# Kernel tuning notes

Measured on AMD Instinct MI355X. Metric: run time of the kernel, lower is better.

## Reference

```python
import jax, jax.numpy as jnp
import numpy as np

B, C, T = 16, 768, 1024
STEPS, NNEG, OFFSET = 12, 10, 1
COPIES = NNEG + 1


def setup_inputs() -> dict:
    key = jax.random.key(0)
    k1, k2, k3, k4 = jax.random.split(key, 4)
    x = jax.random.normal(k1, (B, C, T), jnp.float32)
    y = jax.random.normal(k2, (B, C, T), jnp.float32)
    # ConvTranspose2d(in_dim, out_dim, (1, steps)) weight -> [C_in, C_out, steps]
    W = jax.random.normal(k3, (C, C, STEPS), jnp.float32) * 0.02
    b = jnp.zeros((C,), jnp.float32)
    # Negative-sample indices, replicating torch sample_negatives (sample_distance=None):
    # randint in [0, T-1), bump collisions with the positive timestep, add per-batch offset.
    neg = jax.random.randint(k4, (B, NNEG * T), 0, T - 1)
    tszs = jnp.repeat(jnp.arange(T), NNEG)  # [NNEG*T]
    neg = jnp.where(neg >= tszs[None, :], neg + 1, neg)
    neg = neg + jnp.arange(B)[:, None] * T  # index into flattened [B*T]
    return {"x": x, "y": y, "W": W, "b": b, "neg_idxs": neg}


def reference(x, y, W, b, neg_idxs):
    # project_to_steps: ConvTranspose2d with kernel (1, STEPS) on [B,C,T,1] -> [B,C,T,STEPS]
    proj = jnp.einsum('bct,cds->bdts', x, W) + b[None, :, None, None]

    # gather negatives: y -> [C, B*T], fancy-index, reshape to [NNEG, B, C, T]
    yf = jnp.transpose(y, (1, 0, 2)).reshape(C, B * T)
    negs = yf[:, neg_idxs.reshape(-1)].reshape(C, B, NNEG, T)
    negs = jnp.transpose(negs, (2, 1, 0, 3))  # [NNEG, B, C, T]

    targets = jnp.concatenate([y[None], negs], axis=0)  # [COPIES, B, C, T]

    steps = min(STEPS, T - OFFSET)
    preds = []
    for i in range(steps):  # small fixed loop over prediction steps (ragged slice sizes)
        off = i + OFFSET
        # [T-off, B, COPIES]: dot context at step i with targets shifted by off
        p = jnp.einsum('bct,nbct->tbn', proj[..., :T - off, i], targets[..., off:])
        preds.append(p.reshape(-1))
    predictions = jnp.concatenate(preds).reshape(-1, COPIES)  # infonce logits
    labels = jnp.zeros((predictions.shape[0],), jnp.int32)  # positive is copy 0
    return predictions, labels
```

## Files before the change

### kernel.cpp

```cpp
#include <hip/hip_runtime.h>

typedef __bf16 bf16;
typedef __attribute__((ext_vector_type(8))) __bf16 bf16x8;
typedef __attribute__((ext_vector_type(4))) __bf16 bf16x4;
typedef __attribute__((ext_vector_type(4))) float f32x4;

#define B_ 16
#define C_ 768
#define T_ 1024
#define S_ 12
#define NNEG_ 10
#define NCOPY 11
#define NPRED_ROWS 195360
#define NPRED (NPRED_ROWS * NCOPY)

__device__ __forceinline__ void gload16(const void* g, void* l) {
    __builtin_amdgcn_global_load_lds(
        (__attribute__((address_space(1))) void*)g,
        (__attribute__((address_space(3))) void*)l, 16, 0, 0);
}

__global__ void k_wt(const float* __restrict__ W, bf16* __restrict__ WtT) {
    int id = blockIdx.x * blockDim.x + threadIdx.x;
    if (id >= C_ * C_) return;
    int d = id / C_, c = id % C_;
    const float* src = W + ((size_t)c * C_ + d) * S_;
#pragma unroll
    for (int s = 0; s < S_; ++s)
        WtT[(size_t)s * C_ * C_ + id] = (bf16)src[s];
}

__global__ void k_tr(const float* __restrict__ src, bf16* __restrict__ dst, int b0) {
    __shared__ float tile[32][33];
    int bb = blockIdx.z;
    int b = b0 + bb;
    int c0 = blockIdx.y * 32, t0 = blockIdx.x * 32;
    int tx = threadIdx.x & 31, ty = threadIdx.x >> 5;
#pragma unroll
    for (int i = 0; i < 4; ++i)
        tile[ty + i * 8][tx] = src[((size_t)b * C_ + c0 + ty + i * 8) * T_ + t0 + tx];
    __syncthreads();
#pragma unroll
    for (int i = 0; i < 4; ++i)
        dst[((size_t)bb * T_ + t0 + ty + i * 8) * C_ + c0 + tx] = (bf16)tile[tx][ty + i * 8];
}

__global__ void k_labels(float* __restrict__ out) {
    int i = blockIdx.x * blockDim.x + threadIdx.x;
    if (i < NPRED_ROWS) out[NPRED + i] = 0.0f;
}

__global__ __launch_bounds__(256) void k_gemm(
    const bf16* __restrict__ xTc, const bf16* __restrict__ WtT,
    const float* __restrict__ bias, bf16* __restrict__ P)
{
    const int nblk = blockIdx.x;
    const int tblk = blockIdx.y;
    const int bb   = blockIdx.z;
    const int tid  = threadIdx.x;
    const int wave = tid >> 6, lane = tid & 63;
    const int mw = wave >> 1, nw = wave & 1;
    const int quad = lane >> 4, l15 = lane & 15;

    __shared__ __align__(16) bf16 sA[8][2][64][8];
    __shared__ __align__(16) bf16 sB[8][2][64][8];

    const int colk = quad * 8;
    const int rA0 = nblk * 128 + (2 * wave) * 16 + l15;
    const int rB0 = tblk * 128 + (2 * wave) * 16 + l15;
    const bf16* gA0 = WtT + (size_t)rA0 * C_ + colk;
    const bf16* gA1 = gA0 + (size_t)16 * C_;
    const bf16* gB0 = xTc + ((size_t)bb * T_ + rB0) * C_ + colk;
    const bf16* gB1 = gB0 + (size_t)16 * C_;

    f32x4 acc[4][4] = {};

    for (int k0 = 0; k0 < C_; k0 += 64) {
        __syncthreads();
        gload16(gA0 + k0,      &sA[2 * wave][0][0][0]);
        gload16(gA0 + k0 + 32, &sA[2 * wave][1][0][0]);
        gload16(gA1 + k0,      &sA[2 * wave + 1][0][0][0]);
        gload16(gA1 + k0 + 32, &sA[2 * wave + 1][1][0][0]);
        gload16(gB0 + k0,      &sB[2 * wave][0][0][0]);
        gload16(gB0 + k0 + 32, &sB[2 * wave][1][0][0]);
        gload16(gB1 + k0,      &sB[2 * wave + 1][0][0][0]);
        gload16(gB1 + k0 + 32, &sB[2 * wave + 1][1][0][0]);
        __syncthreads();

#pragma unroll
        for (int ks = 0; ks < 2; ++ks) {
            bf16x8 af[4], bfr[4];
#pragma unroll
            for (int i = 0; i < 4; ++i) af[i]  = *(const bf16x8*)&sA[mw * 4 + i][ks][lane][0];
#pragma unroll
            for (int j = 0; j < 4; ++j) bfr[j] = *(const bf16x8*)&sB[nw * 4 + j][ks][lane][0];
#pragma unroll
            for (int i = 0; i < 4; ++i)
#pragma unroll
                for (int j = 0; j < 4; ++j)
                    acc[i][j] = __builtin_amdgcn_mfma_f32_16x16x32_bf16(af[i], bfr[j], acc[i][j], 0, 0, 0);
        }
    }

#pragma unroll
    for (int i = 0; i < 4; ++i) {
        const int nb = (mw * 4 + i) * 16 + quad * 4;
        const f32x4 bv = *(const f32x4*)&bias[(nblk % 6) * 128 + nb];
#pragma unroll
        for (int j = 0; j < 4; ++j) {
            const int t = tblk * 128 + (nw * 4 + j) * 16 + l15;
            bf16x4 v;
#pragma unroll
            for (int r = 0; r < 4; ++r) v[r] = (bf16)(acc[i][j][r] + bv[r]);
            *(bf16x4*)&P[((size_t)bb * T_ + t) * (size_t)(S_ * C_) + (size_t)nblk * 128 + nb] = v;
        }
    }
}

__global__ __launch_bounds__(256) void k_pred(
    const bf16* __restrict__ P, const bf16* __restrict__ yTc,
    const int* __restrict__ neg, float* __restrict__ out, int b0)
{
    const int widx = (blockIdx.x << 2) + (threadIdx.x >> 6);
    const int lane = threadIdx.x & 63;
    const int bb = widx >> 10, tp = widx & 1023;
    const int b = b0 + bb;
    const int quad = lane >> 4, l15 = lane & 15;

    int sA = l15 < S_ ? l15 : S_ - 1;
    int tA = tp - 1 - sA;
    if (tA < 0) tA = 0;
    const bf16* arow = P + ((size_t)bb * T_ + tA) * (S_ * C_) + sA * C_ + quad * 8;

    int ridx;
    if (l15 == 0)            ridx = bb * T_ + tp;
    else if (l15 < NCOPY)    ridx = neg[(size_t)b * (NNEG_ * T_) + (l15 - 1) * T_ + tp] - b0 * T_;
    else                     ridx = bb * T_ + tp;
    const bf16* brow = yTc + (size_t)ridx * C_ + quad * 8;

    f32x4 acc = {};
#pragma unroll 4
    for (int kt = 0; kt < C_ / 32; ++kt) {
        bf16x8 av = *(const bf16x8*)(arow + kt * 32);
        bf16x8 bv = *(const bf16x8*)(brow + kt * 32);
        acc = __builtin_amdgcn_mfma_f32_16x16x32_bf16(av, bv, acc, 0, 0, 0);
    }

    if (l15 < NCOPY) {
#pragma unroll
        for (int r = 0; r < 4; ++r) {
            int s = quad * 4 + r;
            int t = tp - 1 - s;
            if (s < S_ && t >= 0) {
                int rowbase = s * (T_ - 1) - (s * (s - 1)) / 2;
                out[(((size_t)(rowbase + t)) * B_ + b) * NCOPY + l15] = acc[r];
            }
        }
    }
}

extern "C" void kernel_launch(void* const* d_in, const int* in_sizes, int n_in,
                              void* d_out, int out_size, void* d_ws, size_t ws_size,
                              hipStream_t stream) {
    const float* x    = (const float*)d_in[0];
    const float* y    = (const float*)d_in[1];
    const float* W    = (const float*)d_in[2];
    const float* bias = (const float*)d_in[3];
    const int*   neg  = (const int*)d_in[4];
    float* out = (float*)d_out;

    const size_t offW    = (size_t)S_ * C_ * C_ * 2;
    const size_t perb_xy = (size_t)T_ * C_ * 2;
    const size_t perb_p  = (size_t)T_ * S_ * C_ * 2;
    const size_t perb    = 2 * perb_xy + perb_p;

    int bchunk = (int)((ws_size - offW) / perb);
    if (bchunk < 1) bchunk = 1;
    if (bchunk > B_) bchunk = B_;

    char* ws = (char*)d_ws;
    bf16* WtT = (bf16*)ws;
    bf16* xTc = (bf16*)(ws + offW);
    bf16* yTc = (bf16*)(ws + offW + (size_t)bchunk * perb_xy);
    bf16* P   = (bf16*)(ws + offW + (size_t)bchunk * perb_xy * 2);

    k_wt<<<dim3((C_ * C_ + 255) / 256), 256, 0, stream>>>(W, WtT);
    k_labels<<<dim3((NPRED_ROWS + 255) / 256), 256, 0, stream>>>(out);

    for (int b0 = 0; b0 < B_;) {
        int cb = bchunk < (B_ - b0) ? bchunk : (B_ - b0);
        k_tr<<<dim3(T_ / 32, C_ / 32, cb), 256, 0, stream>>>(x, xTc, b0);
        k_tr<<<dim3(T_ / 32, C_ / 32, cb), 256, 0, stream>>>(y, yTc, b0);
        k_gemm<<<dim3(72, 8, cb), 256, 0, stream>>>(xTc, WtT, bias, P);
        k_pred<<<dim3(cb * 256), 256, 0, stream>>>(P, yTc, neg, out, b0);
        b0 += cb;
    }
}
```

Measured before the change: 745.2 us.

## Use 32x32x16 MFMA in projection GEMM and fuse small launches

The projection GEMM switches from 16x16x32 to 32x32x16 bf16 MFMA tiles with a 2x2 accumulator layout per wave. It halves the k-step to 32 and shrinks the LDS staging buffers to match. The two transpose launches are merged into one grid over x and y, and label zeroing moves into the prediction kernel, so k_labels is no longer launched. This removes launch overhead and aims for better MFMA throughput per LDS read, at the cost of twice as many k-loop barriers.

```diff
diff --git a/kernel.cpp b/kernel.cpp
--- a/kernel.cpp
+++ b/kernel.cpp
@@ -4,6 +4,7 @@
 typedef __attribute__((ext_vector_type(8))) __bf16 bf16x8;
 typedef __attribute__((ext_vector_type(4))) __bf16 bf16x4;
 typedef __attribute__((ext_vector_type(4))) float f32x4;
+typedef __attribute__((ext_vector_type(16))) float f32x16;
 
 #define B_ 16
 #define C_ 768
@@ -30,9 +31,13 @@
         WtT[(size_t)s * C_ * C_ + id] = (bf16)src[s];
 }
 
-__global__ void k_tr(const float* __restrict__ src, bf16* __restrict__ dst, int b0) {
+__global__ void k_tr2(const float* __restrict__ x, const float* __restrict__ y,
+                      bf16* __restrict__ xTc, bf16* __restrict__ yTc, int b0, int cb) {
     __shared__ float tile[32][33];
-    int bb = blockIdx.z;
+    int zz = blockIdx.z;
+    const float* src = (zz < cb) ? x : y;
+    bf16* dst = (zz < cb) ? xTc : yTc;
+    int bb = (zz < cb) ? zz : zz - cb;
     int b = b0 + bb;
     int c0 = blockIdx.y * 32, t0 = blockIdx.x * 32;
     int tx = threadIdx.x & 31, ty = threadIdx.x >> 5;
@@ -45,11 +50,6 @@
         dst[((size_t)bb * T_ + t0 + ty + i * 8) * C_ + c0 + tx] = (bf16)tile[tx][ty + i * 8];
 }
 
-__global__ void k_labels(float* __restrict__ out) {
-    int i = blockIdx.x * blockDim.x + threadIdx.x;
-    if (i < NPRED_ROWS) out[NPRED + i] = 0.0f;
-}
-
 __global__ __launch_bounds__(256) void k_gemm(
     const bf16* __restrict__ xTc, const bf16* __restrict__ WtT,
     const float* __restrict__ bias, bf16* __restrict__ P)
@@ -60,59 +60,53 @@
     const int tid  = threadIdx.x;
     const int wave = tid >> 6, lane = tid & 63;
     const int mw = wave >> 1, nw = wave & 1;
-    const int quad = lane >> 4, l15 = lane & 15;
+    const int l31 = lane & 31, lhi = lane >> 5;
 
-    __shared__ __align__(16) bf16 sA[8][2][64][8];
-    __shared__ __align__(16) bf16 sB[8][2][64][8];
+    __shared__ __align__(16) bf16 sA[4][2][64][8];
+    __shared__ __align__(16) bf16 sB[4][2][64][8];
 
-    const int colk = quad * 8;
-    const int rA0 = nblk * 128 + (2 * wave) * 16 + l15;
-    const int rB0 = tblk * 128 + (2 * wave) * 16 + l15;
-    const bf16* gA0 = WtT + (size_t)rA0 * C_ + colk;
-    const bf16* gA1 = gA0 + (size_t)16 * C_;
-    const bf16* gB0 = xTc + ((size_t)bb * T_ + rB0) * C_ + colk;
-    const bf16* gB1 = gB0 + (size_t)16 * C_;
+    const bf16* gA = WtT + (size_t)(nblk * 128 + wave * 32 + l31) * C_ + lhi * 8;
+    const bf16* gB = xTc + ((size_t)bb * T_ + tblk * 128 + wave * 32 + l31) * C_ + lhi * 8;
 
-    f32x4 acc[4][4] = {};
+    f32x16 acc[2][2] = {};
 
-    for (int k0 = 0; k0 < C_; k0 += 64) {
+    for (int k0 = 0; k0 < C_; k0 += 32) {
         __syncthreads();
-        gload16(gA0 + k0,      &sA[2 * wave][0][0][0]);
-        gload16(gA0 + k0 + 32, &sA[2 * wave][1][0][0]);
-        gload16(gA1 + k0,      &sA[2 * wave + 1][0][0][0]);
-        gload16(gA1 + k0 + 32, &sA[2 * wave + 1][1][0][0]);
-        gload16(gB0 + k0,      &sB[2 * wave][0][0][0]);
-        gload16(gB0 + k0 + 32, &sB[2 * wave][1][0][0]);
-        gload16(gB1 + k0,      &sB[2 * wave + 1][0][0][0]);
-        gload16(gB1 + k0 + 32, &sB[2 * wave + 1][1][0][0]);
+        gload16(gA + k0,      &sA[wave][0][0][0]);
+        gload16(gA + k0 + 16, &sA[wave][1][0][0]);
+        gload16(gB + k0,      &sB[wave][0][0][0]);
+        gload16(gB + k0 + 16, &sB[wave][1][0][0]);
         __syncthreads();
 
 #pragma unroll
         for (int ks = 0; ks < 2; ++ks) {
-            bf16x8 af[4], bfr[4];
+            bf16x8 af[2], bfr[2];
 #pragma unroll
-            for (int i = 0; i < 4; ++i) af[i]  = *(const bf16x8*)&sA[mw * 4 + i][ks][lane][0];
+            for (int i = 0; i < 2; ++i) af[i]  = *(const bf16x8*)&sA[2 * mw + i][ks][lane][0];
 #pragma unroll
-            for (int j = 0; j < 4; ++j) bfr[j] = *(const bf16x8*)&sB[nw * 4 + j][ks][lane][0];
+            for (int j = 0; j < 2; ++j) bfr[j] = *(const bf16x8*)&sB[2 * nw + j][ks][lane][0];
 #pragma unroll
-            for (int i = 0; i < 4; ++i)
+            for (int i = 0; i < 2; ++i)
 #pragma unroll
-                for (int j = 0; j < 4; ++j)
-                    acc[i][j] = __builtin_amdgcn_mfma_f32_16x16x32_bf16(af[i], bfr[j], acc[i][j], 0, 0, 0);
+                for (int j = 0; j < 2; ++j)
+                    acc[i][j] = __builtin_amdgcn_mfma_f32_32x32x16_bf16(af[i], bfr[j], acc[i][j], 0, 0, 0);
         }
     }
 
 #pragma unroll
-    for (int i = 0; i < 4; ++i) {
-        const int nb = (mw * 4 + i) * 16 + quad * 4;
-        const f32x4 bv = *(const f32x4*)&bias[(nblk % 6) * 128 + nb];
+    for (int i = 0; i < 2; ++i) {
 #pragma unroll
-        for (int j = 0; j < 4; ++j) {
-            const int t = tblk * 128 + (nw * 4 + j) * 16 + l15;
-            bf16x4 v;
+        for (int rg = 0; rg < 4; ++rg) {
+            const int dl = mw * 64 + i * 32 + rg * 8 + lhi * 4;
+            const f32x4 bv = *(const f32x4*)&bias[(nblk % 6) * 128 + dl];
 #pragma unroll
-            for (int r = 0; r < 4; ++r) v[r] = (bf16)(acc[i][j][r] + bv[r]);
-            *(bf16x4*)&P[((size_t)bb * T_ + t) * (size_t)(S_ * C_) + (size_t)nblk * 128 + nb] = v;
+            for (int j = 0; j < 2; ++j) {
+                const int t = tblk * 128 + nw * 64 + j * 32 + l31;
+                bf16x4 v;
+#pragma unroll
+                for (int rr = 0; rr < 4; ++rr) v[rr] = (bf16)(acc[i][j][rg * 4 + rr] + bv[rr]);
+                *(bf16x4*)&P[((size_t)bb * T_ + t) * (size_t)(S_ * C_) + (size_t)nblk * 128 + dl] = v;
+            }
         }
     }
 }
@@ -146,15 +140,15 @@
         acc = __builtin_amdgcn_mfma_f32_16x16x32_bf16(av, bv, acc, 0, 0, 0);
     }
 
-    if (l15 < NCOPY) {
 #pragma unroll
-        for (int r = 0; r < 4; ++r) {
-            int s = quad * 4 + r;
-            int t = tp - 1 - s;
-            if (s < S_ && t >= 0) {
-                int rowbase = s * (T_ - 1) - (s * (s - 1)) / 2;
-                out[(((size_t)(rowbase + t)) * B_ + b) * NCOPY + l15] = acc[r];
-            }
+    for (int r = 0; r < 4; ++r) {
+        int s = quad * 4 + r;
+        int t = tp - 1 - s;
+        if (s < S_ && t >= 0) {
+            int rowbase = s * (T_ - 1) - (s * (s - 1)) / 2;
+            size_t row = (size_t)(rowbase + t) * B_ + b;
+            if (l15 < NCOPY)       out[row * NCOPY + l15] = acc[r];
+            else if (l15 == NCOPY) out[NPRED + row] = 0.0f;
         }
     }
 }
@@ -185,12 +179,10 @@
     bf16* P   = (bf16*)(ws + offW + (size_t)bchunk * perb_xy * 2);
 
     k_wt<<<dim3((C_ * C_ + 255) / 256), 256, 0, stream>>>(W, WtT);
-    k_labels<<<dim3((NPRED_ROWS + 255) / 256), 256, 0, stream>>>(out);
 
     for (int b0 = 0; b0 < B_;) {
         int cb = bchunk < (B_ - b0) ? bchunk : (B_ - b0);
-        k_tr<<<dim3(T_ / 32, C_ / 32, cb), 256, 0, stream>>>(x, xTc, b0);
-        k_tr<<<dim3(T_ / 32, C_ / 32, cb), 256, 0, stream>>>(y, yTc, b0);
+        k_tr2<<<dim3(T_ / 32, C_ / 32, 2 * cb), 256, 0, stream>>>(x, y, xTc, yTc, b0, cb);
         k_gemm<<<dim3(72, 8, cb), 256, 0, stream>>>(xTc, WtT, bias, P);
         k_pred<<<dim3(cb * 256), 256, 0, stream>>>(P, yTc, neg, out, b0);
         b0 += cb;
```

After: 753.0 us. Within noise of the previous version (+1.1%).

## Double-buffer GEMM LDS via register prefetch and merge small launches

Applied to the files above, without the earlier changes.

The projection GEMM swaps direct global-to-LDS loads with two syncs per K step for a register-prefetched, double-buffered LDS pipeline. It uses one barrier per 32-wide K step and sets an occupancy hint of 4 blocks per SM. The two transpose launches become one, and the labels zero-fill moves into the prediction kernel's store epilogue, removing launch overhead. The risks are higher register pressure from prefetch registers combined with the occupancy bound, and more barrier iterations with smaller K steps.

```diff
diff --git a/kernel.cpp b/kernel.cpp
--- a/kernel.cpp
+++ b/kernel.cpp
@@ -14,12 +14,6 @@
 #define NPRED_ROWS 195360
 #define NPRED (NPRED_ROWS * NCOPY)
 
-__device__ __forceinline__ void gload16(const void* g, void* l) {
-    __builtin_amdgcn_global_load_lds(
-        (__attribute__((address_space(1))) void*)g,
-        (__attribute__((address_space(3))) void*)l, 16, 0, 0);
-}
-
 __global__ void k_wt(const float* __restrict__ W, bf16* __restrict__ WtT) {
     int id = blockIdx.x * blockDim.x + threadIdx.x;
     if (id >= C_ * C_) return;
@@ -30,9 +24,13 @@
         WtT[(size_t)s * C_ * C_ + id] = (bf16)src[s];
 }
 
-__global__ void k_tr(const float* __restrict__ src, bf16* __restrict__ dst, int b0) {
+__global__ void k_tr2(const float* __restrict__ x, const float* __restrict__ y,
+                      bf16* __restrict__ xTc, bf16* __restrict__ yTc, int b0, int cb) {
     __shared__ float tile[32][33];
-    int bb = blockIdx.z;
+    int zz = blockIdx.z;
+    const float* src = (zz < cb) ? x : y;
+    bf16* dst = (zz < cb) ? xTc : yTc;
+    int bb = (zz < cb) ? zz : zz - cb;
     int b = b0 + bb;
     int c0 = blockIdx.y * 32, t0 = blockIdx.x * 32;
     int tx = threadIdx.x & 31, ty = threadIdx.x >> 5;
@@ -45,12 +43,7 @@
         dst[((size_t)bb * T_ + t0 + ty + i * 8) * C_ + c0 + tx] = (bf16)tile[tx][ty + i * 8];
 }
 
-__global__ void k_labels(float* __restrict__ out) {
-    int i = blockIdx.x * blockDim.x + threadIdx.x;
-    if (i < NPRED_ROWS) out[NPRED + i] = 0.0f;
-}
-
-__global__ __launch_bounds__(256) void k_gemm(
+__global__ __launch_bounds__(256, 4) void k_gemm(
     const bf16* __restrict__ xTc, const bf16* __restrict__ WtT,
     const float* __restrict__ bias, bf16* __restrict__ P)
 {
@@ -62,44 +55,57 @@
     const int mw = wave >> 1, nw = wave & 1;
     const int quad = lane >> 4, l15 = lane & 15;
 
-    __shared__ __align__(16) bf16 sA[8][2][64][8];
-    __shared__ __align__(16) bf16 sB[8][2][64][8];
+    __shared__ __align__(16) bf16 sA[2][8][64][8];
+    __shared__ __align__(16) bf16 sB[2][8][64][8];
 
     const int colk = quad * 8;
-    const int rA0 = nblk * 128 + (2 * wave) * 16 + l15;
-    const int rB0 = tblk * 128 + (2 * wave) * 16 + l15;
-    const bf16* gA0 = WtT + (size_t)rA0 * C_ + colk;
+    const bf16* gA0 = WtT + (size_t)(nblk * 128 + 2 * wave * 16 + l15) * C_ + colk;
     const bf16* gA1 = gA0 + (size_t)16 * C_;
-    const bf16* gB0 = xTc + ((size_t)bb * T_ + rB0) * C_ + colk;
+    const bf16* gB0 = xTc + ((size_t)bb * T_ + tblk * 128 + 2 * wave * 16 + l15) * C_ + colk;
     const bf16* gB1 = gB0 + (size_t)16 * C_;
 
     f32x4 acc[4][4] = {};
 
-    for (int k0 = 0; k0 < C_; k0 += 64) {
+    bf16x8 rA0 = *(const bf16x8*)gA0;
+    bf16x8 rA1 = *(const bf16x8*)gA1;
+    bf16x8 rB0 = *(const bf16x8*)gB0;
+    bf16x8 rB1 = *(const bf16x8*)gB1;
+    *(bf16x8*)&sA[0][2 * wave][lane][0]     = rA0;
+    *(bf16x8*)&sA[0][2 * wave + 1][lane][0] = rA1;
+    *(bf16x8*)&sB[0][2 * wave][lane][0]     = rB0;
+    *(bf16x8*)&sB[0][2 * wave + 1][lane][0] = rB1;
+    rA0 = *(const bf16x8*)(gA0 + 32);
+    rA1 = *(const bf16x8*)(gA1 + 32);
+    rB0 = *(const bf16x8*)(gB0 + 32);
+    rB1 = *(const bf16x8*)(gB1 + 32);
+
+#pragma unroll
+    for (int it = 0; it < C_ / 32; ++it) {
+        const int p = it & 1;
         __syncthreads();
-        gload16(gA0 + k0,      &sA[2 * wave][0][0][0]);
-        gload16(gA0 + k0 + 32, &sA[2 * wave][1][0][0]);
-        gload16(gA1 + k0,      &sA[2 * wave + 1][0][0][0]);
-        gload16(gA1 + k0 + 32, &sA[2 * wave + 1][1][0][0]);
-        gload16(gB0 + k0,      &sB[2 * wave][0][0][0]);
-        gload16(gB0 + k0 + 32, &sB[2 * wave][1][0][0]);
-        gload16(gB1 + k0,      &sB[2 * wave + 1][0][0][0]);
-        gload16(gB1 + k0 + 32, &sB[2 * wave + 1][1][0][0]);
-        __syncthreads();
-
-#pragma unroll
-        for (int ks = 0; ks < 2; ++ks) {
-            bf16x8 af[4], bfr[4];
-#pragma unroll
-            for (int i = 0; i < 4; ++i) af[i]  = *(const bf16x8*)&sA[mw * 4 + i][ks][lane][0];
-#pragma unroll
-            for (int j = 0; j < 4; ++j) bfr[j] = *(const bf16x8*)&sB[nw * 4 + j][ks][lane][0];
-#pragma unroll
-            for (int i = 0; i < 4; ++i)
-#pragma unroll
-                for (int j = 0; j < 4; ++j)
-                    acc[i][j] = __builtin_amdgcn_mfma_f32_16x16x32_bf16(af[i], bfr[j], acc[i][j], 0, 0, 0);
-        }
+        if (it + 1 < C_ / 32) {
+            *(bf16x8*)&sA[p ^ 1][2 * wave][lane][0]     = rA0;
+            *(bf16x8*)&sA[p ^ 1][2 * wave + 1][lane][0] = rA1;
+            *(bf16x8*)&sB[p ^ 1][2 * wave][lane][0]     = rB0;
+            *(bf16x8*)&sB[p ^ 1][2 * wave + 1][lane][0] = rB1;
+        }
+        if (it + 2 < C_ / 32) {
+            const int ko = (it + 2) * 32;
+            rA0 = *(const bf16x8*)(gA0 + ko);
+            rA1 = *(const bf16x8*)(gA1 + ko);
+            rB0 = *(const bf16x8*)(gB0 + ko);
+            rB1 = *(const bf16x8*)(gB1 + ko);
+        }
+        bf16x8 af[4], bfr[4];
+#pragma unroll
+        for (int i = 0; i < 4; ++i) af[i]  = *(const bf16x8*)&sA[p][mw * 4 + i][lane][0];
+#pragma unroll
+        for (int j = 0; j < 4; ++j) bfr[j] = *(const bf16x8*)&sB[p][nw * 4 + j][lane][0];
+#pragma unroll
+        for (int i = 0; i < 4; ++i)
+#pragma unroll
+            for (int j = 0; j < 4; ++j)
+                acc[i][j] = __builtin_amdgcn_mfma_f32_16x16x32_bf16(af[i], bfr[j], acc[i][j], 0, 0, 0);
     }
 
 #pragma unroll
@@ -146,15 +152,15 @@
         acc = __builtin_amdgcn_mfma_f32_16x16x32_bf16(av, bv, acc, 0, 0, 0);
     }
 
-    if (l15 < NCOPY) {
-#pragma unroll
-        for (int r = 0; r < 4; ++r) {
-            int s = quad * 4 + r;
-            int t = tp - 1 - s;
-            if (s < S_ && t >= 0) {
-                int rowbase = s * (T_ - 1) - (s * (s - 1)) / 2;
-                out[(((size_t)(rowbase + t)) * B_ + b) * NCOPY + l15] = acc[r];
-            }
+#pragma unroll
+    for (int r = 0; r < 4; ++r) {
+        int s = quad * 4 + r;
+        int t = tp - 1 - s;
+        if (s < S_ && t >= 0) {
+            int rowbase = s * (T_ - 1) - (s * (s - 1)) / 2;
+            size_t row = (size_t)(rowbase + t) * B_ + b;
+            if (l15 < NCOPY)       out[row * NCOPY + l15] = acc[r];
+            else if (l15 == NCOPY) out[NPRED + row] = 0.0f;
         }
     }
 }
@@ -185,12 +191,10 @@
     bf16* P   = (bf16*)(ws + offW + (size_t)bchunk * perb_xy * 2);
 
     k_wt<<<dim3((C_ * C_ + 255) / 256), 256, 0, stream>>>(W, WtT);
-    k_labels<<<dim3((NPRED_ROWS + 255) / 256), 256, 0, stream>>>(out);
 
     for (int b0 = 0; b0 < B_;) {
         int cb = bchunk < (B_ - b0) ? bchunk : (B_ - b0);
-        k_tr<<<dim3(T_ / 32, C_ / 32, cb), 256, 0, stream>>>(x, xTc, b0);
-        k_tr<<<dim3(T_ / 32, C_ / 32, cb), 256, 0, stream>>>(y, yTc, b0);
+        k_tr2<<<dim3(T_ / 32, C_ / 32, 2 * cb), 256, 0, stream>>>(x, y, xTc, yTc, b0, cb);
         k_gemm<<<dim3(72, 8, cb), 256, 0, stream>>>(xTc, WtT, bias, P);
         k_pred<<<dim3(cb * 256), 256, 0, stream>>>(P, yTc, neg, out, b0);
         b0 += cb;
```

After: 730.5 us. -2.0%, faster.
